# Kernel tuning notes

Hardware: AMD Instinct MI355X
Metric: run time of the kernel (lower is better)

The kernel has to match this reference:

```python
import jax, jax.numpy as jnp
import numpy as np

N_NODES = 100000
N_EDGES = 1600000
IN, HID, OUT = 256, 128, 1


def setup_inputs() -> dict:
    key = jax.random.key(0)
    ks = jax.random.split(key, 12)
    inp = {
        "x": jax.random.normal(ks[0], (N_NODES, IN), dtype=jnp.float32),
        "W_t": jax.random.normal(ks[1], (IN, HID), dtype=jnp.float32) / np.sqrt(IN),
        "b_t": jnp.zeros((HID,), dtype=jnp.float32),
        "W_self0": jax.random.normal(ks[2], (HID, HID), dtype=jnp.float32) / np.sqrt(HID),
        "b_self0": jnp.zeros((HID,), dtype=jnp.float32),
        "W_neigh0": jax.random.normal(ks[3], (HID, HID), dtype=jnp.float32) / np.sqrt(HID),
        "W_self1": jax.random.normal(ks[4], (HID, HID), dtype=jnp.float32) / np.sqrt(HID),
        "b_self1": jnp.zeros((HID,), dtype=jnp.float32),
        "W_neigh1": jax.random.normal(ks[5], (HID, HID), dtype=jnp.float32) / np.sqrt(HID),
        "W_fin": jax.random.normal(ks[6], (HID, OUT), dtype=jnp.float32) / np.sqrt(HID),
        "src": jax.random.randint(ks[7], (N_EDGES,), 0, N_NODES, dtype=jnp.int64 if jax.config.jax_enable_x64 else jnp.int32),
        "dst": jax.random.randint(ks[8], (N_EDGES,), 0, N_NODES, dtype=jnp.int64 if jax.config.jax_enable_x64 else jnp.int32),
    }
    return inp


def _sage_mean_layer(h, src, dst, W_self, b_self, W_neigh):
    # DGL SAGEConv('mean'): fc_self(h_dst) + fc_neigh(mean over in-neighbors)
    msg = h[src]  # [E, H] gather
    summed = jax.ops.segment_sum(msg, dst, num_segments=N_NODES)
    deg = jax.ops.segment_sum(jnp.ones((msg.shape[0],), h.dtype), dst, num_segments=N_NODES)
    h_neigh = summed / jnp.maximum(deg, 1.0)[:, None]
    out = h @ W_self + b_self + h_neigh @ W_neigh
    return jax.nn.relu(out)  # dropout is identity in eval mode


def reference(x, W_t, b_t, W_self0, b_self0, W_neigh0, W_self1, b_self1, W_neigh1, W_fin, src, dst):
    h = x @ W_t + b_t
    h = _sage_mean_layer(h, src, dst, W_self0, b_self0, W_neigh0)
    h = _sage_mean_layer(h, src, dst, W_self1, b_self1, W_neigh1)
    out = h @ W_fin  # [N, 1]
    return out.squeeze()
```

## Files before the change

kernel.cpp:

```cpp
#include <hip/hip_runtime.h>
#include <hip/hip_fp16.h>

#define HIDDEN 128
#define BSHIFT 9
#define NBUCK_MAX 256

using f32x4 = __attribute__((ext_vector_type(4))) float;
using f16x8 = __attribute__((ext_vector_type(8))) _Float16;

__device__ __forceinline__ void gload16(const void* g, void* l) {
    __builtin_amdgcn_global_load_lds((const __attribute__((address_space(1))) void*)g,
                                     (__attribute__((address_space(3))) void*)l,
                                     16, 0, 0);
}

__global__ void zero_ints(int* __restrict__ a, int n) {
    int i = blockIdx.x * 256 + threadIdx.x;
    if (i < n) a[i] = 0;
}

__launch_bounds__(256)
__global__ void bucket_hist(const int* __restrict__ dst, int* __restrict__ bcnt, int e) {
    __shared__ int c[NBUCK_MAX];
    const int t = threadIdx.x;
    c[t] = 0;
    __syncthreads();
    const int tile0 = blockIdx.x * 4096;
    const int end = min(e, tile0 + 4096);
    for (int i = tile0 + t; i < end; i += 256)
        atomicAdd(&c[dst[i] >> BSHIFT], 1);
    __syncthreads();
    if (c[t]) atomicAdd(&bcnt[t], c[t]);
}

__global__ void scan_buckets(const int* __restrict__ bcnt, int* __restrict__ boffs,
                             int* __restrict__ cursor, int nb) {
    __shared__ int sd[256];
    const int t = threadIdx.x;
    int v = (t < nb) ? bcnt[t] : 0;
    sd[t] = v;
    __syncthreads();
    for (int o = 1; o < 256; o <<= 1) {
        int add = (t >= o) ? sd[t - o] : 0;
        __syncthreads();
        sd[t] += add;
        __syncthreads();
    }
    const int ex = sd[t] - v;
    if (t < nb) { boffs[t] = ex; cursor[t] = ex; }
    if (t == nb - 1) boffs[nb] = ex + v;
}

__launch_bounds__(256)
__global__ void partition_pairs(const int* __restrict__ src, const int* __restrict__ dst,
                                int* __restrict__ cursor,
                                unsigned long long* __restrict__ pairs, int e) {
    __shared__ int cnt[NBUCK_MAX];
    __shared__ int base[NBUCK_MAX];
    const int t = threadIdx.x;
    const int tile0 = blockIdx.x * 4096;
    cnt[t] = 0;
    __syncthreads();
    int s[16], d[16], b[16];
    #pragma unroll
    for (int j = 0; j < 16; ++j) {
        const int i = tile0 + j * 256 + t;
        if (i < e) {
            d[j] = dst[i];
            s[j] = src[i];
            b[j] = d[j] >> BSHIFT;
            atomicAdd(&cnt[b[j]], 1);
        } else {
            b[j] = -1;
        }
    }
    __syncthreads();
    const int c = cnt[t];
    base[t] = c ? atomicAdd(&cursor[t], c) : 0;
    __syncthreads();
    cnt[t] = 0;
    __syncthreads();
    #pragma unroll
    for (int j = 0; j < 16; ++j) {
        if (b[j] >= 0) {
            const int r = atomicAdd(&cnt[b[j]], 1);
            pairs[(size_t)base[b[j]] + r] =
                ((unsigned long long)(unsigned)d[j] << 32) | (unsigned)s[j];
        }
    }
}

__launch_bounds__(256)
__global__ void place_csr2(const unsigned long long* __restrict__ pairs,
                           const int* __restrict__ boffs,
                           int* __restrict__ offs, int* __restrict__ csr,
                           int n, int e) {
    __shared__ int cnt[1 << BSHIFT];
    __shared__ int sc[256];
    const int b = blockIdx.x;
    const int t = threadIdx.x;
    const int node0 = b << BSHIFT;
    const int nn = min(1 << BSHIFT, n - node0);
    cnt[t] = 0;
    cnt[t + 256] = 0;
    __syncthreads();
    const int beg = boffs[b], end = boffs[b + 1];
    for (int i = beg + t; i < end; i += 256)
        atomicAdd(&cnt[(int)(pairs[i] >> 32) - node0], 1);
    __syncthreads();
    const int a0 = cnt[2 * t], a1 = cnt[2 * t + 1];
    const int s = a0 + a1;
    sc[t] = s;
    __syncthreads();
    for (int o = 1; o < 256; o <<= 1) {
        int add = (t >= o) ? sc[t - o] : 0;
        __syncthreads();
        sc[t] += add;
        __syncthreads();
    }
    const int g0 = beg + sc[t] - s;
    const int g1 = g0 + a0;
    if (2 * t < nn)     offs[node0 + 2 * t] = g0;
    if (2 * t + 1 < nn) offs[node0 + 2 * t + 1] = g1;
    __syncthreads();
    cnt[2 * t] = g0;
    cnt[2 * t + 1] = g1;
    if (node0 + nn == n && t == 0) offs[n] = e;
    __syncthreads();
    for (int i = beg + t; i < end; i += 256) {
        const unsigned long long pr = pairs[i];
        const int dd = (int)(pr >> 32) - node0;
        const int ss = (int)(unsigned)pr;
        const int p = atomicAdd(&cnt[dd], 1);
        csr[p] = ss;
    }
}

__global__ void pack_weights(const float* __restrict__ W_t, const float* __restrict__ Ws0,
                             const float* __restrict__ Wn0, const float* __restrict__ Ws1,
                             const float* __restrict__ Wn1,
                             __half* p_t, __half* p_l0, __half* p_l1) {
    const int bid = blockIdx.x;
    const float* W; __half* out; int b0; int S0;
    if (bid < 16)      { W = W_t; out = p_t;  b0 = 0;  S0 = 0; }
    else if (bid < 24) { W = Ws0; out = p_l0; b0 = 16; S0 = 0; }
    else if (bid < 32) { W = Wn0; out = p_l0; b0 = 24; S0 = 4; }
    else if (bid < 40) { W = Ws1; out = p_l1; b0 = 32; S0 = 0; }
    else               { W = Wn1; out = p_l1; b0 = 40; S0 = 4; }
    const int idx = (bid - b0) * 256 + threadIdx.x;
    const int step = idx >> 9;
    const int r = idx & 511;
    const int l = r & 63;
    const int col = (r >> 6) * 16 + (l & 15);
    const int k0 = step * 32 + ((l >> 4) << 3);
    const size_t o = (size_t)(S0 + step) * 4096 + (size_t)r * 8;
    #pragma unroll
    for (int j = 0; j < 8; ++j) {
        float f = W[(k0 + j) * HIDDEN + col];
        __half h = __float2half_rn(f);
        out[o + j] = h;
        out[32768 + o + j] = __float2half_rn((f - __half2float(h)) * 32.0f);
    }
}

template <bool RELU, bool FINAL>
__launch_bounds__(256, 8)
__global__ void sage32(const __half* __restrict__ h,
                       const int* __restrict__ offs, const int* __restrict__ csr,
                       const __half* __restrict__ Wp,
                       const float* __restrict__ bias,
                       const float* __restrict__ wfin,
                       void* __restrict__ outv, int nrows) {
    __shared__ __align__(16) __half As[8][2][64][8];
    __shared__ float red[FINAL ? 32 : 1][4];

    const int t = threadIdx.x;
    const int lane = t & 63;
    const int w = t >> 6;
    const int blockRow0 = blockIdx.x * 32;

    {
        const int kk = w * 32 + ((lane >> 4) << 3);
        #pragma unroll
        for (int rt = 0; rt < 2; ++rt) {
            const int row = min(blockRow0 + rt * 16 + (lane & 15), nrows - 1);
            gload16(h + (size_t)row * HIDDEN + kk, &As[w][rt][0][0]);
        }
    }

    {
        const int slot = lane >> 4;
        const int c8 = (lane & 15) * 8;
        #pragma unroll 1
        for (int p = 0; p < 4; ++p) {
            const int rl0 = w * 8 + p * 2;
            const int rl1 = rl0 + 1;
            const int n0 = min(blockRow0 + rl0, nrows - 1);
            const int n1 = min(blockRow0 + rl1, nrows - 1);
            const int s0 = offs[n0];
            const int d0 = offs[n0 + 1] - s0;
            const int s1 = offs[n1];
            const int d1 = offs[n1 + 1] - s1;
            float a0[8] = {0.f, 0.f, 0.f, 0.f, 0.f, 0.f, 0.f, 0.f};
            float a1[8] = {0.f, 0.f, 0.f, 0.f, 0.f, 0.f, 0.f, 0.f};
            const int dmax = max(d0, d1);
            for (int i = slot; i < dmax; i += 16) {
                int idx0[4], idx1[4];
                #pragma unroll
                for (int u = 0; u < 4; ++u) {
                    const int e = i + u * 4;
                    idx0[u] = (e < d0) ? csr[s0 + e] : -1;
                    idx1[u] = (e < d1) ? csr[s1 + e] : -1;
                }
                #pragma unroll
                for (int u = 0; u < 4; ++u) {
                    if (idx0[u] >= 0) {
                        uint4 raw = *(const uint4*)&h[(size_t)idx0[u] * HIDDEN + c8];
                        const __half2* hp = (const __half2*)&raw;
                        #pragma unroll
                        for (int m = 0; m < 4; ++m) {
                            float2 f = __half22float2(hp[m]);
                            a0[2 * m] += f.x;
                            a0[2 * m + 1] += f.y;
                        }
                    }
                    if (idx1[u] >= 0) {
                        uint4 raw = *(const uint4*)&h[(size_t)idx1[u] * HIDDEN + c8];
                        const __half2* hp = (const __half2*)&raw;
                        #pragma unroll
                        for (int m = 0; m < 4; ++m) {
                            float2 f = __half22float2(hp[m]);
                            a1[2 * m] += f.x;
                            a1[2 * m + 1] += f.y;
                        }
                    }
                }
            }
            #pragma unroll
            for (int k = 0; k < 8; ++k) {
                a0[k] += __shfl_xor(a0[k], 16, 64);
                a0[k] += __shfl_xor(a0[k], 32, 64);
                a1[k] += __shfl_xor(a1[k], 16, 64);
                a1[k] += __shfl_xor(a1[k], 32, 64);
            }
            if (slot == 0) {
                const float i0 = 1.0f / (float)max(d0, 1);
                const float i1 = 1.0f / (float)max(d1, 1);
                f16x8 v0, v1;
                #pragma unroll
                for (int j = 0; j < 8; ++j) {
                    v0[j] = (_Float16)(a0[j] * i0);
                    v1[j] = (_Float16)(a1[j] * i1);
                }
                *(f16x8*)&As[4 + (lane >> 2)][rl0 >> 4][(rl0 & 15) + 16 * (lane & 3)][0] = v0;
                *(f16x8*)&As[4 + (lane >> 2)][rl1 >> 4][(rl1 & 15) + 16 * (lane & 3)][0] = v1;
            }
        }
    }
    __syncthreads();

    f32x4 acc[2][2];
    #pragma unroll
    for (int i = 0; i < 2; ++i)
        #pragma unroll
        for (int j = 0; j < 2; ++j) acc[i][j] = (f32x4){0.f, 0.f, 0.f, 0.f};

    const _Float16 S = (_Float16)0.03125f;

    #pragma unroll
    for (int step = 0; step < 8; ++step) {
        const __half* wb = Wp + (size_t)step * 4096 + (w * 2) * 512 + lane * 8;
        f16x8 a[2], asr[2];
        #pragma unroll
        for (int rt = 0; rt < 2; ++rt) {
            a[rt] = *(const f16x8*)&As[step][rt][lane][0];
            asr[rt] = a[rt] * S;
        }
        #pragma unroll
        for (int c2 = 0; c2 < 2; ++c2) {
            f16x8 wh = *(const f16x8*)(wb + c2 * 512);
            f16x8 wl = *(const f16x8*)(wb + 32768 + c2 * 512);
            acc[0][c2] = __builtin_amdgcn_mfma_f32_16x16x32_f16(a[0], wh, acc[0][c2], 0, 0, 0);
            acc[1][c2] = __builtin_amdgcn_mfma_f32_16x16x32_f16(a[1], wh, acc[1][c2], 0, 0, 0);
            acc[0][c2] = __builtin_amdgcn_mfma_f32_16x16x32_f16(asr[0], wl, acc[0][c2], 0, 0, 0);
            acc[1][c2] = __builtin_amdgcn_mfma_f32_16x16x32_f16(asr[1], wl, acc[1][c2], 0, 0, 0);
        }
    }

    if constexpr (FINAL) {
        float part[2][4];
        #pragma unroll
        for (int rt = 0; rt < 2; ++rt)
            #pragma unroll
            for (int j = 0; j < 4; ++j) part[rt][j] = 0.f;
        #pragma unroll
        for (int c2 = 0; c2 < 2; ++c2) {
            const int col = w * 32 + c2 * 16 + (lane & 15);
            const float wf = wfin[col];
            const float bc = bias[col];
            #pragma unroll
            for (int rt = 0; rt < 2; ++rt)
                #pragma unroll
                for (int j = 0; j < 4; ++j) {
                    float v = acc[rt][c2][j] + bc;
                    if (RELU) v = fmaxf(v, 0.f);
                    part[rt][j] = fmaf(v, wf, part[rt][j]);
                }
        }
        #pragma unroll
        for (int o = 1; o < 16; o <<= 1)
            #pragma unroll
            for (int rt = 0; rt < 2; ++rt)
                #pragma unroll
                for (int j = 0; j < 4; ++j)
                    part[rt][j] += __shfl_xor(part[rt][j], o, 64);
        if ((lane & 15) == 0) {
            #pragma unroll
            for (int rt = 0; rt < 2; ++rt)
                #pragma unroll
                for (int j = 0; j < 4; ++j)
                    red[rt * 16 + ((lane >> 4) << 2) + j][w] = part[rt][j];
        }
        __syncthreads();
        if (t < 32) {
            const int r = blockRow0 + t;
            if (r < nrows)
                ((float*)outv)[r] = red[t][0] + red[t][1] + red[t][2] + red[t][3];
        }
    } else {
        __half* out = (__half*)outv;
        #pragma unroll
        for (int c2 = 0; c2 < 2; ++c2) {
            const int col = w * 32 + c2 * 16 + (lane & 15);
            const float bc = bias[col];
            #pragma unroll
            for (int rt = 0; rt < 2; ++rt) {
                const int r0 = blockRow0 + rt * 16 + ((lane >> 4) << 2);
                #pragma unroll
                for (int j = 0; j < 4; ++j) {
                    const int r = r0 + j;
                    if (r < nrows) {
                        float v = acc[rt][c2][j] + bc;
                        if (RELU) v = fmaxf(v, 0.f);
                        out[(size_t)r * HIDDEN + col] = __float2half(v);
                    }
                }
            }
        }
    }
}

__launch_bounds__(256, 8)
__global__ void gemm_xr(const float* __restrict__ X, const __half* __restrict__ Wp,
                        const float* __restrict__ bias,
                        __half* __restrict__ outp, int nrows) {
    __shared__ __align__(16) __half As[8][2][64][8];

    const int t = threadIdx.x;
    const int lane = t & 63;
    const int w = t >> 6;
    const int blockRow0 = blockIdx.x * 32;

    {
        const int kc = (lane >> 4) << 3;
        #pragma unroll
        for (int b = 0; b < 2; ++b) {
            f32x4 v[2][2];
            #pragma unroll
            for (int i = 0; i < 2; ++i) {
                const int sid = w + (b * 2 + i) * 4;
                const int step = sid >> 1, rt = sid & 1;
                const int r = min(blockRow0 + rt * 16 + (lane & 15), nrows - 1);
                const float* p = X + (size_t)r * 256 + step * 32 + kc;
                v[i][0] = *(const f32x4*)p;
                v[i][1] = *(const f32x4*)(p + 4);
            }
            #pragma unroll
            for (int i = 0; i < 2; ++i) {
                const int sid = w + (b * 2 + i) * 4;
                const int step = sid >> 1, rt = sid & 1;
                f16x8 hh;
                #pragma unroll
                for (int j = 0; j < 4; ++j) hh[j] = (_Float16)v[i][0][j];
                #pragma unroll
                for (int j = 0; j < 4; ++j) hh[4 + j] = (_Float16)v[i][1][j];
                *(f16x8*)&As[step][rt][lane][0] = hh;
            }
        }
    }
    __syncthreads();

    f32x4 acc[2][2];
    #pragma unroll
    for (int i = 0; i < 2; ++i)
        #pragma unroll
        for (int j = 0; j < 2; ++j) acc[i][j] = (f32x4){0.f, 0.f, 0.f, 0.f};

    const _Float16 S = (_Float16)0.03125f;

    #pragma unroll
    for (int step = 0; step < 8; ++step) {
        const __half* wb = Wp + (size_t)step * 4096 + (w * 2) * 512 + lane * 8;
        f16x8 a[2], asr[2];
        #pragma unroll
        for (int rt = 0; rt < 2; ++rt) {
            a[rt] = *(const f16x8*)&As[step][rt][lane][0];
            asr[rt] = a[rt] * S;
        }
        #pragma unroll
        for (int c2 = 0; c2 < 2; ++c2) {
            f16x8 wh = *(const f16x8*)(wb + c2 * 512);
            f16x8 wl = *(const f16x8*)(wb + 32768 + c2 * 512);
            acc[0][c2] = __builtin_amdgcn_mfma_f32_16x16x32_f16(a[0], wh, acc[0][c2], 0, 0, 0);
            acc[1][c2] = __builtin_amdgcn_mfma_f32_16x16x32_f16(a[1], wh, acc[1][c2], 0, 0, 0);
            acc[0][c2] = __builtin_amdgcn_mfma_f32_16x16x32_f16(asr[0], wl, acc[0][c2], 0, 0, 0);
            acc[1][c2] = __builtin_amdgcn_mfma_f32_16x16x32_f16(asr[1], wl, acc[1][c2], 0, 0, 0);
        }
    }

    #pragma unroll
    for (int c2 = 0; c2 < 2; ++c2) {
        const int col = w * 32 + c2 * 16 + (lane & 15);
        const float bc = bias[col];
        #pragma unroll
        for (int rt = 0; rt < 2; ++rt) {
            const int r0 = blockRow0 + rt * 16 + ((lane >> 4) << 2);
            #pragma unroll
            for (int j = 0; j < 4; ++j) {
                const int r = r0 + j;
                if (r < nrows)
                    outp[(size_t)r * HIDDEN + col] = __float2half(acc[rt][c2][j] + bc);
            }
        }
    }
}

extern "C" void kernel_launch(void* const* d_in, const int* in_sizes, int n_in,
                              void* d_out, int out_size, void* d_ws, size_t ws_size,
                              hipStream_t stream) {
    const float* x     = (const float*)d_in[0];
    const float* W_t   = (const float*)d_in[1];
    const float* b_t   = (const float*)d_in[2];
    const float* W_s0  = (const float*)d_in[3];
    const float* b_s0  = (const float*)d_in[4];
    const float* W_n0  = (const float*)d_in[5];
    const float* W_s1  = (const float*)d_in[6];
    const float* b_s1  = (const float*)d_in[7];
    const float* W_n1  = (const float*)d_in[8];
    const float* W_fin = (const float*)d_in[9];
    const int*   src   = (const int*)d_in[10];
    const int*   dst   = (const int*)d_in[11];
    float* out = (float*)d_out;

    const int N = in_sizes[0] / 256;
    const int E = in_sizes[10];

    size_t off_b = 0;
    auto carve = [&](size_t bytes) {
        size_t cur = off_b;
        off_b = (off_b + bytes + 255) & ~(size_t)255;
        return cur;
    };
    char* base = (char*)d_ws;
    int* offs   = (int*)(base + carve((size_t)(N + 1) * 4));
    int* bcnt   = (int*)(base + carve(NBUCK_MAX * 4));
    int* boffs  = (int*)(base + carve((NBUCK_MAX + 1) * 4));
    int* cursor = (int*)(base + carve(NBUCK_MAX * 4));
    int* csr    = (int*)(base + carve((size_t)E * 4));
    unsigned long long* pairs = (unsigned long long*)(base + carve((size_t)E * 8));
    __half* wp_t  = (__half*)(base + carve((size_t)65536 * 2));
    __half* wp_l0 = (__half*)(base + carve((size_t)65536 * 2));
    __half* wp_l1 = (__half*)(base + carve((size_t)65536 * 2));
    __half* hA  = (__half*)(base + carve((size_t)N * HIDDEN * 2));
    __half* hB  = (__half*)(base + carve((size_t)N * HIDDEN * 2));
    (void)ws_size; (void)n_in; (void)out_size;

    const int nBuck = (N + (1 << BSHIFT) - 1) >> BSHIFT;

    hipLaunchKernelGGL(zero_ints, dim3(1), dim3(256), 0, stream, bcnt, NBUCK_MAX);
    hipLaunchKernelGGL(bucket_hist, dim3((E + 4095) / 4096), dim3(256), 0, stream, dst, bcnt, E);
    hipLaunchKernelGGL(scan_buckets, dim3(1), dim3(256), 0, stream, bcnt, boffs, cursor, nBuck);
    hipLaunchKernelGGL(partition_pairs, dim3((E + 4095) / 4096), dim3(256), 0, stream,
                       src, dst, cursor, pairs, E);
    hipLaunchKernelGGL(place_csr2, dim3(nBuck), dim3(256), 0, stream, pairs, boffs, offs, csr, N, E);

    hipLaunchKernelGGL(pack_weights, dim3(48), dim3(256), 0, stream,
                       W_t, W_s0, W_n0, W_s1, W_n1, wp_t, wp_l0, wp_l1);

    const int g32 = (N + 31) / 32;

    hipLaunchKernelGGL(gemm_xr, dim3(g32), dim3(256), 0, stream,
                       x, wp_t, b_t, hA, N);
    hipLaunchKernelGGL((sage32<true, false>), dim3(g32), dim3(256), 0, stream,
                       hA, offs, csr, wp_l0, b_s0, (const float*)nullptr, (void*)hB, N);
    hipLaunchKernelGGL((sage32<true, true>), dim3(g32), dim3(256), 0, stream,
                       hB, offs, csr, wp_l1, b_s1, W_fin, (void*)out, N);
}
```

Baseline: 271.0 us.

## Process two row tiles per block in input GEMM with prefetch overlap

The input projection kernel now handles two 32-row tiles per block. It prefetches the second tile's fp32 rows into registers while the MFMA compute for the first tile runs, then converts them and computes. This is meant to hide global load latency, at the cost of more registers (launch bounds drop to 4 waves) and half the grid size. The sage32 kernel's minimum-blocks hint also changes from 8 to 6, giving the compiler more register room at possible occupancy cost.

```diff
diff --git a/kernel.cpp b/kernel.cpp
--- a/kernel.cpp
+++ b/kernel.cpp
@@ -164,7 +164,7 @@
 }
 
 template <bool RELU, bool FINAL>
-__launch_bounds__(256, 8)
+__launch_bounds__(256, 6)
 __global__ void sage32(const __half* __restrict__ h,
                        const int* __restrict__ offs, const int* __restrict__ csr,
                        const __half* __restrict__ Wp,
@@ -350,88 +350,101 @@
     }
 }
 
-__launch_bounds__(256, 8)
-__global__ void gemm_xr(const float* __restrict__ X, const __half* __restrict__ Wp,
+__launch_bounds__(256, 4)
+__global__ void gemm_xp(const float* __restrict__ X, const __half* __restrict__ Wp,
                         const float* __restrict__ bias,
-                        __half* __restrict__ outp, int nrows) {
+                        __half* __restrict__ outp, int nrows, int ntiles) {
     __shared__ __align__(16) __half As[8][2][64][8];
 
     const int t = threadIdx.x;
     const int lane = t & 63;
     const int w = t >> 6;
-    const int blockRow0 = blockIdx.x * 32;
-
-    {
-        const int kc = (lane >> 4) << 3;
-        #pragma unroll
-        for (int b = 0; b < 2; ++b) {
-            f32x4 v[2][2];
-            #pragma unroll
-            for (int i = 0; i < 2; ++i) {
-                const int sid = w + (b * 2 + i) * 4;
-                const int step = sid >> 1, rt = sid & 1;
-                const int r = min(blockRow0 + rt * 16 + (lane & 15), nrows - 1);
-                const float* p = X + (size_t)r * 256 + step * 32 + kc;
-                v[i][0] = *(const f32x4*)p;
-                v[i][1] = *(const f32x4*)(p + 4);
-            }
-            #pragma unroll
-            for (int i = 0; i < 2; ++i) {
-                const int sid = w + (b * 2 + i) * 4;
-                const int step = sid >> 1, rt = sid & 1;
-                f16x8 hh;
-                #pragma unroll
-                for (int j = 0; j < 4; ++j) hh[j] = (_Float16)v[i][0][j];
-                #pragma unroll
-                for (int j = 0; j < 4; ++j) hh[4 + j] = (_Float16)v[i][1][j];
-                *(f16x8*)&As[step][rt][lane][0] = hh;
-            }
-        }
-    }
-    __syncthreads();
-
-    f32x4 acc[2][2];
-    #pragma unroll
-    for (int i = 0; i < 2; ++i)
-        #pragma unroll
-        for (int j = 0; j < 2; ++j) acc[i][j] = (f32x4){0.f, 0.f, 0.f, 0.f};
-
+    const int kc = (lane >> 4) << 3;
     const _Float16 S = (_Float16)0.03125f;
 
-    #pragma unroll
-    for (int step = 0; step < 8; ++step) {
-        const __half* wb = Wp + (size_t)step * 4096 + (w * 2) * 512 + lane * 8;
-        f16x8 a[2], asr[2];
-        #pragma unroll
-        for (int rt = 0; rt < 2; ++rt) {
-            a[rt] = *(const f16x8*)&As[step][rt][lane][0];
-            asr[rt] = a[rt] * S;
+    auto loadT = [&](int tile, f32x4 (&v)[4][2]) {
+        const int br = tile * 32;
+        #pragma unroll
+        for (int s = 0; s < 4; ++s) {
+            const int sid = w + s * 4;
+            const int step = sid >> 1, rt = sid & 1;
+            const int r = min(br + rt * 16 + (lane & 15), nrows - 1);
+            const float* p = X + (size_t)r * 256 + step * 32 + kc;
+            v[s][0] = *(const f32x4*)p;
+            v[s][1] = *(const f32x4*)(p + 4);
+        }
+    };
+    auto writeT = [&](f32x4 (&v)[4][2]) {
+        #pragma unroll
+        for (int s = 0; s < 4; ++s) {
+            const int sid = w + s * 4;
+            const int step = sid >> 1, rt = sid & 1;
+            f16x8 hh;
+            #pragma unroll
+            for (int j = 0; j < 4; ++j) hh[j] = (_Float16)v[s][0][j];
+            #pragma unroll
+            for (int j = 0; j < 4; ++j) hh[4 + j] = (_Float16)v[s][1][j];
+            *(f16x8*)&As[step][rt][lane][0] = hh;
+        }
+    };
+    auto computeStore = [&](int tile) {
+        const int br = tile * 32;
+        f32x4 acc[2][2];
+        #pragma unroll
+        for (int i = 0; i < 2; ++i)
+            #pragma unroll
+            for (int j = 0; j < 2; ++j) acc[i][j] = (f32x4){0.f, 0.f, 0.f, 0.f};
+        #pragma unroll
+        for (int step = 0; step < 8; ++step) {
+            const __half* wb = Wp + (size_t)step * 4096 + (w * 2) * 512 + lane * 8;
+            f16x8 a[2], asr[2];
+            #pragma unroll
+            for (int rt = 0; rt < 2; ++rt) {
+                a[rt] = *(const f16x8*)&As[step][rt][lane][0];
+                asr[rt] = a[rt] * S;
+            }
+            #pragma unroll
+            for (int c2 = 0; c2 < 2; ++c2) {
+                f16x8 wh = *(const f16x8*)(wb + c2 * 512);
+                f16x8 wl = *(const f16x8*)(wb + 32768 + c2 * 512);
+                acc[0][c2] = __builtin_amdgcn_mfma_f32_16x16x32_f16(a[0], wh, acc[0][c2], 0, 0, 0);
+                acc[1][c2] = __builtin_amdgcn_mfma_f32_16x16x32_f16(a[1], wh, acc[1][c2], 0, 0, 0);
+                acc[0][c2] = __builtin_amdgcn_mfma_f32_16x16x32_f16(asr[0], wl, acc[0][c2], 0, 0, 0);
+                acc[1][c2] = __builtin_amdgcn_mfma_f32_16x16x32_f16(asr[1], wl, acc[1][c2], 0, 0, 0);
+            }
         }
         #pragma unroll
         for (int c2 = 0; c2 < 2; ++c2) {
-            f16x8 wh = *(const f16x8*)(wb + c2 * 512);
-            f16x8 wl = *(const f16x8*)(wb + 32768 + c2 * 512);
-            acc[0][c2] = __builtin_amdgcn_mfma_f32_16x16x32_f16(a[0], wh, acc[0][c2], 0, 0, 0);
-            acc[1][c2] = __builtin_amdgcn_mfma_f32_16x16x32_f16(a[1], wh, acc[1][c2], 0, 0, 0);
-            acc[0][c2] = __builtin_amdgcn_mfma_f32_16x16x32_f16(asr[0], wl, acc[0][c2], 0, 0, 0);
-            acc[1][c2] = __builtin_amdgcn_mfma_f32_16x16x32_f16(asr[1], wl, acc[1][c2], 0, 0, 0);
-        }
-    }
-
-    #pragma unroll
-    for (int c2 = 0; c2 < 2; ++c2) {
-        const int col = w * 32 + c2 * 16 + (lane & 15);
-        const float bc = bias[col];
-        #pragma unroll
-        for (int rt = 0; rt < 2; ++rt) {
-            const int r0 = blockRow0 + rt * 16 + ((lane >> 4) << 2);
-            #pragma unroll
-            for (int j = 0; j < 4; ++j) {
-                const int r = r0 + j;
-                if (r < nrows)
-                    outp[(size_t)r * HIDDEN + col] = __float2half(acc[rt][c2][j] + bc);
-            }
-        }
+            const int col = w * 32 + c2 * 16 + (lane & 15);
+            const float bc = bias[col];
+            #pragma unroll
+            for (int rt = 0; rt < 2; ++rt) {
+                const int r0 = br + rt * 16 + ((lane >> 4) << 2);
+                #pragma unroll
+                for (int j = 0; j < 4; ++j) {
+                    const int r = r0 + j;
+                    if (r < nrows)
+                        outp[(size_t)r * HIDDEN + col] = __float2half(acc[rt][c2][j] + bc);
+                }
+            }
+        }
+    };
+
+    const int t0 = blockIdx.x * 2;
+    const int t1 = t0 + 1;
+    const bool has1 = (t1 < ntiles);
+
+    f32x4 vA[4][2], vB[4][2];
+    loadT(t0, vA);
+    writeT(vA);
+    __syncthreads();
+    if (has1) loadT(t1, vB);
+    computeStore(t0);
+    if (has1) {
+        __syncthreads();
+        writeT(vB);
+        __syncthreads();
+        computeStore(t1);
     }
 }
 
@@ -487,10 +500,12 @@
     hipLaunchKernelGGL(pack_weights, dim3(48), dim3(256), 0, stream,
                        W_t, W_s0, W_n0, W_s1, W_n1, wp_t, wp_l0, wp_l1);
 
-    const int g32 = (N + 31) / 32;
-
-    hipLaunchKernelGGL(gemm_xr, dim3(g32), dim3(256), 0, stream,
-                       x, wp_t, b_t, hA, N);
+    const int ntiles = (N + 31) / 32;
+    const int g32 = ntiles;
+    const int gx = (ntiles + 1) / 2;
+
+    hipLaunchKernelGGL(gemm_xp, dim3(gx), dim3(256), 0, stream,
+                       x, wp_t, b_t, hA, N, ntiles);
     hipLaunchKernelGGL((sage32<true, false>), dim3(g32), dim3(256), 0, stream,
                        hA, offs, csr, wp_l0, b_s0, (const float*)nullptr, (void*)hB, N);
     hipLaunchKernelGGL((sage32<true, true>), dim3(g32), dim3(256), 0, stream,
```

After: 270.9 us. No clear change (-0.1%).
